# Kernel tuning notes

Hardware: AMD Instinct MI355X
Metric: run time of the kernel (lower is better)

The kernel has to match this reference:

```python
import jax, jax.numpy as jnp
from jax import lax
import numpy as np

H, W = 4096, 4096
KERNEL_SIZES = [3, 5, 7, 9, 11, 13, 15]


def setup_inputs() -> dict:
    key = jax.random.key(0)
    k1, k2 = jax.random.split(key)
    x = jax.random.uniform(k1, (H, W), dtype=jnp.float32)
    base_map = jax.random.uniform(k2, (H, W), dtype=jnp.float32)
    return {"x": x, "base_map": base_map}


def _box_blur(x4, k):
    # replicate ('edge') padding by k//2, then VALID conv with uniform 1/k^2 kernel
    p = k // 2
    xp = jnp.pad(x4, ((0, 0), (0, 0), (p, p), (p, p)), mode='edge')
    w = jnp.full((1, 1, k, k), 1.0 / (k * k), dtype=x4.dtype)
    return lax.conv_general_dilated(
        xp, w, window_strides=(1, 1), padding='VALID',
        dimension_numbers=('NCHW', 'OIHW', 'NCHW'))


def reference(x, base_map):
    # x: [H, W] -> [1, 1, H, W]
    x4 = x[None, None, :, :]
    acc = jnp.zeros_like(x4)
    for k in KERNEL_SIZES:  # fixed small set of structurally distinct convs
        acc = acc + _box_blur(x4, k)
    out = (acc / len(KERNEL_SIZES)) * base_map[None, None, :, :]
    return out  # [1, 1, H, W]
```

## Files before the change

### kernel.cpp

```cpp
#include <hip/hip_runtime.h>

typedef __attribute__((ext_vector_type(2))) float f32x2;

#define W 4096
#define H 4096
#define NT 128
#define COLS 256
#define SR 32
#define GROUP 4
#define NSTAGE (SR + 14)
#define NG 12
#define LW 288
#define RAD 7
#define PEND 18

__device__ __forceinline__ void gl_lds16(float* lds, const float* g) {
    __builtin_amdgcn_global_load_lds(
        (const __attribute__((address_space(1))) void*)g,
        (__attribute__((address_space(3))) void*)lds, 16, 0, 0);
}
__device__ __forceinline__ void gl_lds4(float* lds, const float* g) {
    __builtin_amdgcn_global_load_lds(
        (const __attribute__((address_space(1))) void*)g,
        (__attribute__((address_space(3))) void*)lds, 4, 0, 0);
}

__global__ __launch_bounds__(NT, 4) void multibox_kernel(
    const float* __restrict__ x, const float* __restrict__ base,
    float* __restrict__ out)
{
    __shared__ float buf[2][GROUP][LW];

    const int t  = threadIdx.x;
    const int w  = t >> 6;
    const int l  = t & 63;
    const int c0 = blockIdx.x * COLS;
    const int i0 = blockIdx.y * SR;

    const float w3  = 1.f/(7.f*9.f);
    const float w5  = 1.f/(7.f*25.f);
    const float w7  = 1.f/(7.f*49.f);
    const float w9  = 1.f/(7.f*81.f);
    const float w11 = 1.f/(7.f*121.f);
    const float w13 = 1.f/(7.f*169.f);
    const float w15 = 1.f/(7.f*225.f);

    const int colL = min(max(c0 -   8 +     l, 0), W - 1);
    const int colM =         c0 +  56 + 4 * l;
    const int colR = min(    c0 + 248 +     l,     W - 1);

    auto stage = [&](int g, int b) {
#pragma unroll
        for (int k = 0; k < 2; ++k) {
            const int rr = w + 2 * k;
            const int rc = min(max(i0 - RAD + g * GROUP + rr, 0), H - 1);
            const float* rp = x + (size_t)rc * W;
            float* lb = &buf[b][rr][0];
            gl_lds4(lb, rp + colL);
            if (l < 48) gl_lds16(lb +  64, rp + colM);
            if (l < 16) gl_lds4 (lb + 256, rp + colR);
        }
    };

    f32x2 Pnd[PEND];
#pragma unroll
    for (int q = 0; q < PEND; ++q) Pnd[q] = f32x2{0.f, 0.f};

    auto compute_group = [&](int b, int g) {
#pragma unroll
        for (int rr = 0; rr < GROUP; ++rr) {
            if (g * GROUP + rr < NSTAGE) {
                const float* p = &buf[b][rr][2 * t];
                f32x2 q2[9];
#pragma unroll
                for (int i = 0; i < 9; ++i) q2[i] = *(const f32x2*)(p + 2 * i);

                auto PR = [&](int a) -> f32x2 {
                    if ((a & 1) == 0) return q2[a / 2];
                    f32x2 r;
                    r.x = q2[a / 2].y;
                    r.y = q2[a / 2 + 1].x;
                    return r;
                };

                f32x2 s3  = PR(7) + PR(8) + PR(9);
                f32x2 s5  = s3  + PR(6) + PR(10);
                f32x2 s7  = s5  + PR(5) + PR(11);
                f32x2 s9  = s7  + PR(4) + PR(12);
                f32x2 s11 = s9  + PR(3) + PR(13);
                f32x2 s13 = s11 + PR(2) + PR(14);
                f32x2 s15 = s13 + PR(1) + PR(15);

                f32x2 c7 = f32x2{w15, w15} * s15;
                f32x2 c6 = c7 + f32x2{w13, w13} * s13;
                f32x2 c5 = c6 + f32x2{w11, w11} * s11;
                f32x2 c4 = c5 + f32x2{w9 , w9 } * s9;
                f32x2 c3 = c4 + f32x2{w7 , w7 } * s7;
                f32x2 c2 = c3 + f32x2{w5 , w5 } * s5;
                f32x2 c1 = c2 + f32x2{w3 , w3 } * s3;

                Pnd[rr +  0] += c7; Pnd[rr +  1] += c6; Pnd[rr +  2] += c5;
                Pnd[rr +  3] += c4; Pnd[rr +  4] += c3; Pnd[rr +  5] += c2;
                Pnd[rr +  6] += c1; Pnd[rr +  7] += c1; Pnd[rr +  8] += c1;
                Pnd[rr +  9] += c2; Pnd[rr + 10] += c3; Pnd[rr + 11] += c4;
                Pnd[rr + 12] += c5; Pnd[rr + 13] += c6; Pnd[rr + 14] += c7;
            }
        }

#pragma unroll
        for (int p = 0; p < GROUP; ++p) {
            const int o_ofs = 4 * g - 14 + p;
            if (o_ofs >= 0 && o_ofs < SR) {
                const size_t bi = (size_t)(i0 + o_ofs) * W + c0 + 2 * t;
                f32x2 bm = *(const f32x2*)(base + bi);
                f32x2 ov = Pnd[p] * bm;
                *(f32x2*)(out + bi) = ov;
            }
        }

#pragma unroll
        for (int p = 0; p < PEND - GROUP; ++p) Pnd[p] = Pnd[p + GROUP];
#pragma unroll
        for (int p = PEND - GROUP; p < PEND; ++p) Pnd[p] = f32x2{0.f, 0.f};
    };

    stage(0, 0);
    __syncthreads();

#pragma clang loop unroll(disable)
    for (int g = 0; g < NG - 1; ++g) {
        stage(g + 1, (g + 1) & 1);
        compute_group(g & 1, g);
        __syncthreads();
    }
    compute_group((NG - 1) & 1, NG - 1);
}

extern "C" void kernel_launch(void* const* d_in, const int* in_sizes, int n_in,
                              void* d_out, int out_size, void* d_ws, size_t ws_size,
                              hipStream_t stream) {
    const float* x    = (const float*)d_in[0];
    const float* base = (const float*)d_in[1];
    float* out        = (float*)d_out;

    dim3 grid(W / COLS, H / SR);
    multibox_kernel<<<grid, dim3(NT), 0, stream>>>(x, base, out);
}
```

Before: 48.76 us.

## Compute four columns per thread with wider tiles and shorter row strips

Each thread now produces four output columns instead of two, so a block covers 512 columns and the LDS row width grows to 528. The row strip per block drops from 32 to 16, giving 8 staged groups instead of 12, and occupancy is lowered to 3 blocks. The aim is to amortize LDS reads and the horizontal sums across more outputs and to use 16-byte global stores, at the cost of more registers per thread. Shorter strips also raise the vertical halo overhead, since 30 input rows are now loaded for every 16 output rows.

```diff
diff --git a/kernel.cpp b/kernel.cpp
--- a/kernel.cpp
+++ b/kernel.cpp
@@ -5,12 +5,12 @@
 #define W 4096
 #define H 4096
 #define NT 128
-#define COLS 256
-#define SR 32
+#define COLS 512
+#define SR 16
 #define GROUP 4
 #define NSTAGE (SR + 14)
-#define NG 12
-#define LW 288
+#define NG 8
+#define LW 528
 #define RAD 7
 #define PEND 18
 
@@ -25,7 +25,7 @@
         (__attribute__((address_space(3))) void*)lds, 4, 0, 0);
 }
 
-__global__ __launch_bounds__(NT, 4) void multibox_kernel(
+__global__ __launch_bounds__(NT, 3) void multibox_kernel(
     const float* __restrict__ x, const float* __restrict__ base,
     float* __restrict__ out)
 {
@@ -36,6 +36,7 @@
     const int l  = t & 63;
     const int c0 = blockIdx.x * COLS;
     const int i0 = blockIdx.y * SR;
+    const int j  = c0 + 4 * t;
 
     const float w3  = 1.f/(7.f*9.f);
     const float w5  = 1.f/(7.f*25.f);
@@ -45,9 +46,10 @@
     const float w13 = 1.f/(7.f*169.f);
     const float w15 = 1.f/(7.f*225.f);
 
-    const int colL = min(max(c0 -   8 +     l, 0), W - 1);
-    const int colM =         c0 +  56 + 4 * l;
-    const int colR = min(    c0 + 248 +     l,     W - 1);
+    const int colL  = min(max(c0 -   8 +     l, 0), W - 1);
+    const int colM1 =         c0 +  56 + 4 * l;
+    const int colM2 =         c0 + 312 + 4 * l;
+    const int colR  = min(    c0 + 504 +     l,     W - 1);
 
     auto stage = [&](int g, int b) {
 #pragma unroll
@@ -57,53 +59,77 @@
             const float* rp = x + (size_t)rc * W;
             float* lb = &buf[b][rr][0];
             gl_lds4(lb, rp + colL);
-            if (l < 48) gl_lds16(lb +  64, rp + colM);
-            if (l < 16) gl_lds4 (lb + 256, rp + colR);
+            gl_lds16(lb + 64, rp + colM1);
+            if (l < 48) gl_lds16(lb + 320, rp + colM2);
+            if (l < 16) gl_lds4 (lb + 512, rp + colR);
         }
     };
 
-    f32x2 Pnd[PEND];
+    f32x2 PndA[PEND], PndB[PEND];
 #pragma unroll
-    for (int q = 0; q < PEND; ++q) Pnd[q] = f32x2{0.f, 0.f};
+    for (int q = 0; q < PEND; ++q) { PndA[q] = f32x2{0.f, 0.f}; PndB[q] = f32x2{0.f, 0.f}; }
 
     auto compute_group = [&](int b, int g) {
 #pragma unroll
         for (int rr = 0; rr < GROUP; ++rr) {
             if (g * GROUP + rr < NSTAGE) {
-                const float* p = &buf[b][rr][2 * t];
-                f32x2 q2[9];
-#pragma unroll
-                for (int i = 0; i < 9; ++i) q2[i] = *(const f32x2*)(p + 2 * i);
+                const float* p = &buf[b][rr][4 * t];
+                float4 v0 = *(const float4*)(p);
+                float4 v1 = *(const float4*)(p + 4);
+                float4 v2 = *(const float4*)(p + 8);
+                float4 v3 = *(const float4*)(p + 12);
+                float4 v4 = *(const float4*)(p + 16);
+                float f[20];
+                f[0]=v0.x; f[1]=v0.y; f[2]=v0.z; f[3]=v0.w;
+                f[4]=v1.x; f[5]=v1.y; f[6]=v1.z; f[7]=v1.w;
+                f[8]=v2.x; f[9]=v2.y; f[10]=v2.z; f[11]=v2.w;
+                f[12]=v3.x; f[13]=v3.y; f[14]=v3.z; f[15]=v3.w;
+                f[16]=v4.x; f[17]=v4.y; f[18]=v4.z; f[19]=v4.w;
 
-                auto PR = [&](int a) -> f32x2 {
-                    if ((a & 1) == 0) return q2[a / 2];
-                    f32x2 r;
-                    r.x = q2[a / 2].y;
-                    r.y = q2[a / 2 + 1].x;
-                    return r;
+                auto PA = [&](int a) -> f32x2 {
+                    f32x2 r; r.x = f[a]; r.y = f[a + 1]; return r;
                 };
 
-                f32x2 s3  = PR(7) + PR(8) + PR(9);
-                f32x2 s5  = s3  + PR(6) + PR(10);
-                f32x2 s7  = s5  + PR(5) + PR(11);
-                f32x2 s9  = s7  + PR(4) + PR(12);
-                f32x2 s11 = s9  + PR(3) + PR(13);
-                f32x2 s13 = s11 + PR(2) + PR(14);
-                f32x2 s15 = s13 + PR(1) + PR(15);
+                f32x2 sA3  = PA(7) + PA(8) + PA(9);
+                f32x2 sA5  = sA3  + PA(6) + PA(10);
+                f32x2 sA7  = sA5  + PA(5) + PA(11);
+                f32x2 sA9  = sA7  + PA(4) + PA(12);
+                f32x2 sA11 = sA9  + PA(3) + PA(13);
+                f32x2 sA13 = sA11 + PA(2) + PA(14);
+                f32x2 sA15 = sA13 + PA(1) + PA(15);
+                f32x2 sB3  = PA(9)  + PA(10) + PA(11);
+                f32x2 sB5  = sB3  + PA(8) + PA(12);
+                f32x2 sB7  = sB5  + PA(7) + PA(13);
+                f32x2 sB9  = sB7  + PA(6) + PA(14);
+                f32x2 sB11 = sB9  + PA(5) + PA(15);
+                f32x2 sB13 = sB11 + PA(4) + PA(16);
+                f32x2 sB15 = sB13 + PA(3) + PA(17);
 
-                f32x2 c7 = f32x2{w15, w15} * s15;
-                f32x2 c6 = c7 + f32x2{w13, w13} * s13;
-                f32x2 c5 = c6 + f32x2{w11, w11} * s11;
-                f32x2 c4 = c5 + f32x2{w9 , w9 } * s9;
-                f32x2 c3 = c4 + f32x2{w7 , w7 } * s7;
-                f32x2 c2 = c3 + f32x2{w5 , w5 } * s5;
-                f32x2 c1 = c2 + f32x2{w3 , w3 } * s3;
+                f32x2 cA7 = f32x2{w15, w15} * sA15;
+                f32x2 cA6 = cA7 + f32x2{w13, w13} * sA13;
+                f32x2 cA5 = cA6 + f32x2{w11, w11} * sA11;
+                f32x2 cA4 = cA5 + f32x2{w9 , w9 } * sA9;
+                f32x2 cA3 = cA4 + f32x2{w7 , w7 } * sA7;
+                f32x2 cA2 = cA3 + f32x2{w5 , w5 } * sA5;
+                f32x2 cA1 = cA2 + f32x2{w3 , w3 } * sA3;
+                f32x2 cB7 = f32x2{w15, w15} * sB15;
+                f32x2 cB6 = cB7 + f32x2{w13, w13} * sB13;
+                f32x2 cB5 = cB6 + f32x2{w11, w11} * sB11;
+                f32x2 cB4 = cB5 + f32x2{w9 , w9 } * sB9;
+                f32x2 cB3 = cB4 + f32x2{w7 , w7 } * sB7;
+                f32x2 cB2 = cB3 + f32x2{w5 , w5 } * sB5;
+                f32x2 cB1 = cB2 + f32x2{w3 , w3 } * sB3;
 
-                Pnd[rr +  0] += c7; Pnd[rr +  1] += c6; Pnd[rr +  2] += c5;
-                Pnd[rr +  3] += c4; Pnd[rr +  4] += c3; Pnd[rr +  5] += c2;
-                Pnd[rr +  6] += c1; Pnd[rr +  7] += c1; Pnd[rr +  8] += c1;
-                Pnd[rr +  9] += c2; Pnd[rr + 10] += c3; Pnd[rr + 11] += c4;
-                Pnd[rr + 12] += c5; Pnd[rr + 13] += c6; Pnd[rr + 14] += c7;
+                PndA[rr +  0] += cA7; PndA[rr +  1] += cA6; PndA[rr +  2] += cA5;
+                PndA[rr +  3] += cA4; PndA[rr +  4] += cA3; PndA[rr +  5] += cA2;
+                PndA[rr +  6] += cA1; PndA[rr +  7] += cA1; PndA[rr +  8] += cA1;
+                PndA[rr +  9] += cA2; PndA[rr + 10] += cA3; PndA[rr + 11] += cA4;
+                PndA[rr + 12] += cA5; PndA[rr + 13] += cA6; PndA[rr + 14] += cA7;
+                PndB[rr +  0] += cB7; PndB[rr +  1] += cB6; PndB[rr +  2] += cB5;
+                PndB[rr +  3] += cB4; PndB[rr +  4] += cB3; PndB[rr +  5] += cB2;
+                PndB[rr +  6] += cB1; PndB[rr +  7] += cB1; PndB[rr +  8] += cB1;
+                PndB[rr +  9] += cB2; PndB[rr + 10] += cB3; PndB[rr + 11] += cB4;
+                PndB[rr + 12] += cB5; PndB[rr + 13] += cB6; PndB[rr + 14] += cB7;
             }
         }
 
@@ -111,17 +137,21 @@
         for (int p = 0; p < GROUP; ++p) {
             const int o_ofs = 4 * g - 14 + p;
             if (o_ofs >= 0 && o_ofs < SR) {
-                const size_t bi = (size_t)(i0 + o_ofs) * W + c0 + 2 * t;
-                f32x2 bm = *(const f32x2*)(base + bi);
-                f32x2 ov = Pnd[p] * bm;
-                *(f32x2*)(out + bi) = ov;
+                const size_t bi = (size_t)(i0 + o_ofs) * W + j;
+                float4 bm = *(const float4*)(base + bi);
+                float4 ov;
+                ov.x = PndA[p].x * bm.x;
+                ov.y = PndA[p].y * bm.y;
+                ov.z = PndB[p].x * bm.z;
+                ov.w = PndB[p].y * bm.w;
+                *(float4*)(out + bi) = ov;
             }
         }
 
 #pragma unroll
-        for (int p = 0; p < PEND - GROUP; ++p) Pnd[p] = Pnd[p + GROUP];
+        for (int p = 0; p < PEND - GROUP; ++p) { PndA[p] = PndA[p + GROUP]; PndB[p] = PndB[p + GROUP]; }
 #pragma unroll
-        for (int p = PEND - GROUP; p < PEND; ++p) Pnd[p] = f32x2{0.f, 0.f};
+        for (int p = PEND - GROUP; p < PEND; ++p) { PndA[p] = f32x2{0.f, 0.f}; PndB[p] = f32x2{0.f, 0.f}; }
     };
 
     stage(0, 0);
```

Measured after the change: 89.56 us. 83.7% more time.
